# Optimization experiments

Hardware: AMD Instinct MI355X
Metric: run time of the kernel (lower is better)

## Reference

```python
import jax, jax.numpy as jnp
import numpy as np

B, L, H, NH, HD, M, NL, V, RD, NS = 4, 512, 768, 12, 64, 3072, 6, 32000, 128, 2
EPS = 1e-12
COEF = 1.0 / float(np.sqrt(HD))
NEG_INF = float('-inf')


def _ln(x, scale, bias):
    x = x - jnp.mean(x, axis=-1, keepdims=True)
    x = x * jax.lax.rsqrt(jnp.mean(jnp.square(x), axis=-1, keepdims=True) + EPS)
    return x * scale + bias


def setup_inputs() -> dict:
    key = jax.random.key(0)
    ks = jax.random.split(key, 16)
    def p(k, shape):
        return jax.random.normal(k, shape, jnp.float32) * 0.02
    return dict(
        token_ids=jax.random.randint(ks[0], (B, L), 0, V, jnp.int32),
        segment_ids=jax.random.randint(ks[1], (B, L), 0, NS, jnp.int32),
        input_mask=jnp.ones((B, L), jnp.int32),
        tok_emb=p(ks[2], (V, H)),
        seg_emb=p(ks[3], (NS, H)),
        emb_scale=jnp.ones((H,), jnp.float32),
        emb_bias=jnp.zeros((H,), jnp.float32),
        Wq=p(ks[4], (NL, H, NH, HD)), bq=jnp.zeros((NL, NH, HD), jnp.float32),
        Wk=p(ks[5], (NL, H, NH, HD)), bk=jnp.zeros((NL, NH, HD), jnp.float32),
        Wv=p(ks[6], (NL, H, NH, HD)), bv=jnp.zeros((NL, NH, HD), jnp.float32),
        relpos=p(ks[7], (NL, 2 * RD - 1, H)),
        Wo=p(ks[8], (NL, NH, HD, H)), bo=jnp.zeros((NL, H), jnp.float32),
        ln1_s=jnp.ones((NL, H), jnp.float32), ln1_b=jnp.zeros((NL, H), jnp.float32),
        W1=p(ks[9], (NL, H, M)), b1=jnp.zeros((NL, M), jnp.float32),
        W2=p(ks[10], (NL, M, H)), b2=jnp.zeros((NL, H), jnp.float32),
        ln2_s=jnp.ones((NL, H), jnp.float32), ln2_b=jnp.zeros((NL, H), jnp.float32),
    )


def _encoder(token_ids, segment_ids, input_mask,
             tok_emb, seg_emb, emb_scale, emb_bias,
             Wq, bq, Wk, bk, Wv, bv, relpos, Wo, bo,
             ln1_s, ln1_b, W1, b1, W2, b2, ln2_s, ln2_b):
    # Embedding block: token + segment embeddings, layer norm (dropout = eval/no-op)
    x = tok_emb[token_ids] + seg_emb[segment_ids]            # [B, L, H]
    x = _ln(x, emb_scale, emb_bias)
    mask = jnp.where(input_mask.astype(bool), 0.0, NEG_INF)[:, None, None, :]  # [B,1,1,L]

    for i in range(NL):
        # --- relative-position self-attention ---
        q = jnp.einsum('bqe,ehd->bqhd', x, Wq[i]) + bq[i]
        k = jnp.einsum('bke,ehd->bkhd', x, Wk[i]) + bk[i]
        v = jnp.einsum('bke,ehd->bkhd', x, Wv[i]) + bv[i]
        att = jnp.einsum('bqhd,bkhd->bhqk', q, k) + mask      # [B,NH,L,L]
        # skew trick: embed absolute [L,L] scores into relative [L, 2L-1] layout
        att = jnp.pad(att, [(0, 0), (0, 0), (0, 0), (0, L - 2)], constant_values=NEG_INF)
        att = att.reshape(att.shape[:2] + (L * (2 * L - 2),))
        att = jnp.pad(att, [(0, 0), (0, 0), (L - 1, 1)], constant_values=NEG_INF)
        att = att.reshape(att.shape[:2] + (L, 2 * L - 1))     # [B,NH,L,2L-1]
        # relative-position key/value embeddings, edge-padded to 2L-1 rows
        pad = L - RD
        rel_emb = jnp.pad(relpos[i], [(pad, pad), (0, 0)], mode='edge')  # [2L-1, H]
        k_rel = jnp.einsum('re,ehd->rhd', rel_emb, Wk[i]) + bk[i]
        att = (att + jnp.einsum('bqhd,rhd->bhqr', q, k_rel)) * COEF
        probs = jax.nn.softmax(att, axis=-1)                  # [B,NH,L,2L-1]
        v_rel = jnp.einsum('re,ehd->rhd', rel_emb, Wv[i]) + bv[i]
        rel_ctx = jnp.einsum('bhqr,rhd->bqhd', probs, v_rel)
        # un-skew probs back to [B,NH,L,L] for the absolute-position context
        p = probs.reshape(probs.shape[:2] + (L * (2 * L - 1),))[:, :, L - 1:-1]
        p = p.reshape(probs.shape[:2] + (L, 2 * L - 2))[:, :, :, :L]
        ctx = jnp.einsum('bhqk,bkhd->bqhd', p, v) + rel_ctx
        y = jnp.einsum('bqhd,hde->bqe', ctx, Wo[i]) + bo[i]
        x = _ln(x + y, ln1_s[i], ln1_b[i])
        # --- MLP block ---
        y = jax.nn.gelu(jnp.einsum('bqe,em->bqm', x, W1[i]) + b1[i])
        y = jnp.einsum('bqm,me->bqe', y, W2[i]) + b2[i]
        x = _ln(x + y, ln2_s[i], ln2_b[i])
    return x


def reference(token_ids, segment_ids, input_mask,
              tok_emb, seg_emb, emb_scale, emb_bias,
              Wq, bq, Wk, bk, Wv, bv, relpos, Wo, bo,
              ln1_s, ln1_b, W1, b1, W2, b2, ln2_s, ln2_b):
    return _encoder(token_ids, segment_ids, input_mask,
                    tok_emb, seg_emb, emb_scale, emb_bias,
                    Wq, bq, Wk, bk, Wv, bv, relpos, Wo, bo,
                    ln1_s, ln1_b, W1, b1, W2, b2, ln2_s, ln2_b)
```

## Files before the change

kernel.cpp:

```cpp
#include <hip/hip_runtime.h>
#include <hip/hip_bf16.h>
#include <math.h>

#define B_   4
#define L_   512
#define H_   768
#define NH_  12
#define HD_  64
#define M_   3072
#define NL_  6
#define RD_  128
#define NR_  255
#define ROWS (B_*L_)
#define MEXT 2304
#define COEF_ 0.125f

typedef __attribute__((ext_vector_type(8))) short bf16x8;
typedef __attribute__((ext_vector_type(4))) float f32x4;


static __device__ __forceinline__ float wave_reduce_sum(float v) {
#pragma unroll
    for (int off = 32; off > 0; off >>= 1) v += __shfl_xor(v, off, 64);
    return v;
}

static __device__ __forceinline__ float gelu_f(float x) {
    float x3 = x * x * x;
    return 0.5f * x * (1.f + tanhf(0.7978845608028654f * (x + 0.044715f * x3)));
}

static __device__ __forceinline__ unsigned short f2bfu(float v) {
    __hip_bfloat16 h = __float2bfloat16(v);
    return *(unsigned short*)&h;
}

static __device__ __forceinline__ float bfu2f(unsigned short u) {
    union { float f; unsigned int i; } x;
    x.i = ((unsigned int)u) << 16;
    return x.f;
}

static __device__ __forceinline__ void gload16(const void* g, void* l) {
    __builtin_amdgcn_global_load_lds(
        (const __attribute__((address_space(1))) void*)g,
        (__attribute__((address_space(3))) void*)l,
        16, 0, 0);
}


__global__ __launch_bounds__(256) void embed_ln_kernel(
    const int* __restrict__ tok, const int* __restrict__ seg,
    const float* __restrict__ temb, const float* __restrict__ semb,
    const float* __restrict__ sc, const float* __restrict__ bi,
    float* __restrict__ out, __hip_bfloat16* __restrict__ outb)
{
    int row = blockIdx.x;
    int t = threadIdx.x;
    int tid = tok[row], sid = seg[row];
    const float* tp = temb + (size_t)tid * H_;
    const float* sp = semb + (size_t)sid * H_;
    float v[3];
#pragma unroll
    for (int j = 0; j < 3; j++) { int idx = t + j * 256; v[j] = tp[idx] + sp[idx]; }

    __shared__ float red[4];
    __shared__ float bc;
    int lane = t & 63, wid = t >> 6;

    float s = v[0] + v[1] + v[2];
    s = wave_reduce_sum(s);
    if (lane == 0) red[wid] = s;
    __syncthreads();
    if (t == 0) bc = (red[0] + red[1] + red[2] + red[3]) * (1.f / H_);
    __syncthreads();
    float mean = bc;

    float c[3]; float ss = 0.f;
#pragma unroll
    for (int j = 0; j < 3; j++) { c[j] = v[j] - mean; ss += c[j] * c[j]; }
    ss = wave_reduce_sum(ss);
    __syncthreads();
    if (lane == 0) red[wid] = ss;
    __syncthreads();
    if (t == 0) bc = rsqrtf((red[0] + red[1] + red[2] + red[3]) * (1.f / H_) + 1e-12f);
    __syncthreads();
    float r = bc;
#pragma unroll
    for (int j = 0; j < 3; j++) {
        int idx = t + j * 256;
        float o = c[j] * r * sc[idx] + bi[idx];
        out[(size_t)row * H_ + idx] = o;
        outb[(size_t)row * H_ + idx] = __float2bfloat16(o);
    }
}


__global__ __launch_bounds__(256) void add_ln_kernel(
    const float* __restrict__ x, const float* __restrict__ p0,
    const float* __restrict__ p1, const float* __restrict__ p2,
    const float* __restrict__ bias,
    const float* __restrict__ sc, const float* __restrict__ bi,
    float* __restrict__ out, __hip_bfloat16* __restrict__ outb)
{
    int row = blockIdx.x;
    int t = threadIdx.x;
    const float* xp = x + (size_t)row * H_;
    const float* q0 = p0 + (size_t)row * H_;
    const float* q1 = p1 ? p1 + (size_t)row * H_ : nullptr;
    const float* q2 = p2 ? p2 + (size_t)row * H_ : nullptr;
    float v[3];
#pragma unroll
    for (int j = 0; j < 3; j++) {
        int idx = t + j * 256;
        float a = xp[idx] + q0[idx];
        if (q1) a += q1[idx];
        if (q2) a += q2[idx];
        if (bias) a += bias[idx];
        v[j] = a;
    }

    __shared__ float red[4];
    __shared__ float bc;
    int lane = t & 63, wid = t >> 6;

    float s = v[0] + v[1] + v[2];
    s = wave_reduce_sum(s);
    if (lane == 0) red[wid] = s;
    __syncthreads();
    if (t == 0) bc = (red[0] + red[1] + red[2] + red[3]) * (1.f / H_);
    __syncthreads();
    float mean = bc;

    float c[3]; float ss = 0.f;
#pragma unroll
    for (int j = 0; j < 3; j++) { c[j] = v[j] - mean; ss += c[j] * c[j]; }
    ss = wave_reduce_sum(ss);
    __syncthreads();
    if (lane == 0) red[wid] = ss;
    __syncthreads();
    if (t == 0) bc = rsqrtf((red[0] + red[1] + red[2] + red[3]) * (1.f / H_) + 1e-12f);
    __syncthreads();
    float r = bc;
#pragma unroll
    for (int j = 0; j < 3; j++) {
        int idx = t + j * 256;
        float o = c[j] * r * sc[idx] + bi[idx];
        out[(size_t)row * H_ + idx] = o;
        if (outb) outb[(size_t)row * H_ + idx] = __float2bfloat16(o);
    }
}


__global__ __launch_bounds__(256) void pack_layer_kernel(
    const float* __restrict__ wq, const float* __restrict__ wk, const float* __restrict__ wv,
    const float* __restrict__ wo, const float* __restrict__ w1, const float* __restrict__ w2,
    const float* __restrict__ bqL, const float* __restrict__ bkL, const float* __restrict__ bvL,
    const float* __restrict__ relL,
    __hip_bfloat16* __restrict__ WtQ, __hip_bfloat16* __restrict__ WtO,
    __hip_bfloat16* __restrict__ WtW1, __hip_bfloat16* __restrict__ WtW2,
    float* __restrict__ qkvbias, __hip_bfloat16* __restrict__ relb)
{
    const int z = blockIdx.z;
    const int t = threadIdx.x;
    if (z == 6) {
        int id = blockIdx.y * 96 + blockIdx.x;
        if (id < 765) {
            int i = id * 256 + t;
            relb[i] = __float2bfloat16(relL[i]);
        } else if (id < 774) {
            int i = (id - 765) * 256 + t;
            if (i < 2304)
                qkvbias[i] = i < 768 ? bqL[i] : (i < 1536 ? bkL[i - 768] : bvL[i - 1536]);
        }
        return;
    }
    const float* in; __hip_bfloat16* out; int K, N;
    int bx = blockIdx.x, by = blockIdx.y;
    if (z < 4) {
        if (bx >= 24) return;
        K = 768; N = 768;
        in = (z == 0) ? wq : (z == 1) ? wk : (z == 2) ? wv : wo;
        out = (z < 3) ? WtQ + (size_t)z * H_ * H_ : WtO;
    } else if (z == 4) {
        K = 768; N = 3072; in = w1; out = WtW1;
    } else {
        K = 3072; N = 768; in = w2; out = WtW2;
        int tmp = bx; bx = by; by = tmp;
    }
    __shared__ float tile[32][33];
    int bX = bx * 32, bY = by * 32;
    int tx = t & 31, ty = t >> 5;
#pragma unroll
    for (int i = 0; i < 4; i++)
        tile[ty + 8 * i][tx] = in[(size_t)(bY + ty + 8 * i) * N + bX + tx];
    __syncthreads();
#pragma unroll
    for (int i = 0; i < 4; i++)
        out[(size_t)(bX + ty + 8 * i) * K + bY + tx] = __float2bfloat16(tile[tx][ty + 8 * i]);
}


__global__ __launch_bounds__(256) void transpose_vvr_kernel(
    const __hip_bfloat16* __restrict__ qkvb,
    __hip_bfloat16* __restrict__ vT, __hip_bfloat16* __restrict__ vrT)
{
    __shared__ unsigned short tile[64][72];
    const int bx = blockIdx.x;
    const int h  = blockIdx.y;
    const int t = threadIdx.x;
    const int r = t >> 2, c0 = (t & 3) * 16;
    if (bx < 32) {
        const int kb = bx * 64;
        const unsigned short* src = (const unsigned short*)qkvb + (size_t)(kb + r) * 2304 + 1536 + h * 64 + c0;
        *(uint4*)&tile[r][c0]     = *(const uint4*)src;
        *(uint4*)&tile[r][c0 + 8] = *(const uint4*)(src + 8);
        __syncthreads();
        unsigned short outv[16];
#pragma unroll
        for (int i = 0; i < 16; i++) outv[i] = tile[c0 + i][r];
        unsigned short* dst = (unsigned short*)vT +
            ((size_t)((kb >> 9) * NH_ + h) * 64 + r) * 512 + (kb & 511) + c0;
        *(uint4*)dst       = *(uint4*)&outv[0];
        *(uint4*)(dst + 8) = *(uint4*)&outv[8];
    } else {
        const int jb = (bx - 32) * 64;
        const int j = jb + r;
        if (j < NR_) {
            const unsigned short* src = (const unsigned short*)qkvb + (size_t)(2048 + j) * 2304 + 1536 + h * 64 + c0;
            *(uint4*)&tile[r][c0]     = *(const uint4*)src;
            *(uint4*)&tile[r][c0 + 8] = *(const uint4*)(src + 8);
        } else {
#pragma unroll
            for (int i = 0; i < 16; i++) tile[r][c0 + i] = 0;
        }
        __syncthreads();
        unsigned short outv[16];
#pragma unroll
        for (int i = 0; i < 16; i++) outv[i] = tile[c0 + i][r];
        unsigned short* dst = (unsigned short*)vrT + ((size_t)(h * 64) + r) * 256 + jb + c0;
        *(uint4*)dst       = *(uint4*)&outv[0];
        *(uint4*)(dst + 8) = *(uint4*)&outv[8];
    }
}


#define TK 64

__global__ __launch_bounds__(512, 6) void gemm_bf16_kernel(
    const __hip_bfloat16* __restrict__ A, const __hip_bfloat16* __restrict__ Bt,
    const float* __restrict__ bias, float* __restrict__ Cf, __hip_bfloat16* __restrict__ Cb,
    float* __restrict__ CfX, size_t xstride,
    int M, int N, int K, int act, int ksplit)
{
    __shared__ __hip_bfloat16 As[2][128 * TK];
    __shared__ __hip_bfloat16 Bs[2][64 * TK];
    const int t = threadIdx.x;
    const int lane = t & 63;
    const int wid = t >> 6;
    const int lq = lane & 15, lg = lane >> 4;
    const int wm = (wid & 3) * 32, wn = (wid >> 2) * 32;

    const int nbx = gridDim.x;
    const int nwg = nbx * gridDim.y;
    int wgid = blockIdx.y * nbx + blockIdx.x;
    if ((nwg & 7) == 0) { int qq = nwg >> 3; wgid = (wgid & 7) * qq + (wgid >> 3); }
    const int bm = (wgid / nbx) * 128, bn = (wgid % nbx) * 64;
    const int kbase = blockIdx.z * ksplit;

    f32x4 acc[2][2];
#pragma unroll
    for (int i = 0; i < 2; i++)
#pragma unroll
        for (int j = 0; j < 2; j++) acc[i][j] = (f32x4){0.f, 0.f, 0.f, 0.f};

    const int rl = t >> 3;
    const int cswz = (((t & 7) * 16) ^ ((rl & 7) << 4)) >> 1;
    const __hip_bfloat16* ga[2];
    const __hip_bfloat16* gb;
    int lofsA[2], lofsB;
#pragma unroll
    for (int c = 0; c < 2; c++) {
        int rowa = bm + c * 64 + rl; if (rowa >= M) rowa = M - 1;
        ga[c] = A + (size_t)rowa * K + kbase + cswz;
        lofsA[c] = (c * 64 + wid * 8) * TK;
    }
    gb = Bt + (size_t)(bn + rl) * K + kbase + cswz;
    lofsB = (wid * 8) * TK;

    const int nt = ksplit / TK;
    gload16(ga[0], &As[0][lofsA[0]]);
    gload16(ga[1], &As[0][lofsA[1]]);
    gload16(gb,    &Bs[0][lofsB]);
    __syncthreads();

    int cur = 0;
    for (int kt = 0; kt < nt; kt++) {
        if (kt + 1 < nt) {
            const int koff = (kt + 1) * TK;
            gload16(ga[0] + koff, &As[cur ^ 1][lofsA[0]]);
            gload16(ga[1] + koff, &As[cur ^ 1][lofsA[1]]);
            gload16(gb + koff,    &Bs[cur ^ 1][lofsB]);
        }
#pragma unroll
        for (int kh = 0; kh < 2; kh++) {
            const int kb = kh * 64 + lg * 16;
            bf16x8 af[2], bfr[2];
#pragma unroll
            for (int i = 0; i < 2; i++) {
                int ra = wm + i * 16 + lq;
                af[i] = *(const bf16x8*)((const char*)&As[cur][0] + ra * 128 + (kb ^ ((ra & 7) << 4)));
            }
#pragma unroll
            for (int j = 0; j < 2; j++) {
                int rb = wn + j * 16 + lq;
                bfr[j] = *(const bf16x8*)((const char*)&Bs[cur][0] + rb * 128 + (kb ^ ((rb & 7) << 4)));
            }
#pragma unroll
            for (int i = 0; i < 2; i++)
#pragma unroll
                for (int j = 0; j < 2; j++)
                    acc[i][j] = __builtin_amdgcn_mfma_f32_16x16x32_bf16(af[i], bfr[j], acc[i][j], 0, 0, 0);
        }
        __syncthreads();
        cur ^= 1;
    }

    float* outf = (blockIdx.z == 0) ? Cf : (CfX + (size_t)(blockIdx.z - 1) * xstride);
#pragma unroll
    for (int i = 0; i < 2; i++) {
#pragma unroll
        for (int j = 0; j < 2; j++) {
            int col = bn + wn + j * 16 + lq;
            float bsv = bias ? bias[col] : 0.f;
            int row0 = bm + wm + i * 16 + lg * 4;
#pragma unroll
            for (int rr = 0; rr < 4; rr++) {
                int row = row0 + rr;
                if (row >= M) continue;
                float v = acc[i][j][rr] + bsv;
                if (act) v = gelu_f(v);
                if (Cb && blockIdx.z == 0) Cb[(size_t)row * N + col] = __float2bfloat16(v);
                else                       outf[(size_t)row * N + col] = v;
            }
        }
    }
}


#define PS_LD 520
#define PR_LD 264

__global__ __launch_bounds__(256, 3) void attn_kernel(
    const __hip_bfloat16* __restrict__ qkvb,
    const __hip_bfloat16* __restrict__ vT,
    const __hip_bfloat16* __restrict__ vrT,
    const int* __restrict__ mask,
    __hip_bfloat16* __restrict__ ctxb)
{
    __shared__ unsigned short RqPrel[32 * PR_LD];
    __shared__ unsigned short Ps[32 * PS_LD];
    __shared__ float mstat[32 * 4];
    __shared__ float sstat[32 * 4];
    __shared__ float maskb[512];

    const int i_ = blockIdx.x;
    const int c_ = i_ & 7, s_ = i_ >> 3;
    const int p_ = c_ + 8 * (s_ >> 4);
    const int qt = s_ & 15;
    const int b = p_ / 12, h = p_ % 12;

    const int t = threadIdx.x;
    const int lane = t & 63, w = t >> 6;
    const int lq = lane & 15, lg = lane >> 4;

    maskb[t]       = mask[b * L_ + t]       ? 0.f : -1e30f;
    maskb[t + 256] = mask[b * L_ + t + 256] ? 0.f : -1e30f;

    const char* Qbase  = (const char*)qkvb + ((size_t)(b * L_ + qt * 32) * 2304 + h * 64) * 2;
    const char* Kbase  = (const char*)qkvb + ((size_t)(b * L_) * 2304 + 768 + h * 64) * 2;
    const char* KRbase = (const char*)qkvb + ((size_t)2048 * 2304 + 768 + h * 64) * 2;

    bf16x8 afq[2][2];
#pragma unroll
    for (int ks = 0; ks < 2; ks++) {
        const int kofs = ks * 64 + lg * 16;
        afq[ks][0] = *(const bf16x8*)(Qbase + (size_t)lq * 4608 + kofs);
        afq[ks][1] = *(const bf16x8*)(Qbase + (size_t)(16 + lq) * 4608 + kofs);
    }

    {
        f32x4 accr[2][4];
#pragma unroll
        for (int i = 0; i < 2; i++)
#pragma unroll
            for (int j = 0; j < 4; j++) accr[i][j] = (f32x4){0.f, 0.f, 0.f, 0.f};
#pragma unroll
        for (int ks = 0; ks < 2; ks++) {
            const int kofs = ks * 64 + lg * 16;
            bf16x8 bkr_[4];
#pragma unroll
            for (int jt = 0; jt < 4; jt++) {
                int j = w * 64 + jt * 16 + lq;
                int jr = j > 254 ? 254 : j;
                bkr_[jt] = *(const bf16x8*)(KRbase + (size_t)jr * 4608 + kofs);
            }
#pragma unroll
            for (int jt = 0; jt < 4; jt++) {
                accr[0][jt] = __builtin_amdgcn_mfma_f32_16x16x32_bf16(afq[ks][0], bkr_[jt], accr[0][jt], 0, 0, 0);
                accr[1][jt] = __builtin_amdgcn_mfma_f32_16x16x32_bf16(afq[ks][1], bkr_[jt], accr[1][jt], 0, 0, 0);
            }
        }
#pragma unroll
        for (int it = 0; it < 2; it++)
#pragma unroll
            for (int jt = 0; jt < 4; jt++)
#pragma unroll
                for (int r = 0; r < 4; r++)
                    RqPrel[(it * 16 + lg * 4 + r) * PR_LD + w * 64 + jt * 16 + lq] = f2bfu(accr[it][jt][r]);
    }
    __syncthreads();

    f32x4 accs[2][8];
#pragma unroll
    for (int i = 0; i < 2; i++)
#pragma unroll
        for (int j = 0; j < 8; j++) accs[i][j] = (f32x4){0.f, 0.f, 0.f, 0.f};
#pragma unroll
    for (int ks = 0; ks < 2; ks++) {
        const int kofs = ks * 64 + lg * 16;
        bf16x8 bk_[8];
#pragma unroll
        for (int jt = 0; jt < 8; jt++) {
            int key = w * 128 + jt * 16 + lq;
            bk_[jt] = *(const bf16x8*)(Kbase + (size_t)key * 4608 + kofs);
        }
#pragma unroll
        for (int jt = 0; jt < 8; jt++) {
            accs[0][jt] = __builtin_amdgcn_mfma_f32_16x16x32_bf16(afq[ks][0], bk_[jt], accs[0][jt], 0, 0, 0);
            accs[1][jt] = __builtin_amdgcn_mfma_f32_16x16x32_bf16(afq[ks][1], bk_[jt], accs[1][jt], 0, 0, 0);
        }
    }

#pragma unroll
    for (int it = 0; it < 2; it++) {
#pragma unroll
        for (int r = 0; r < 4; r++) {
            int q = it * 16 + lg * 4 + r;
            int qg = qt * 32 + q;
            float mx = -INFINITY;
#pragma unroll
            for (int jt = 0; jt < 8; jt++) {
                int k = w * 128 + jt * 16 + lq;
                int jc = k - qg + 127;
                jc = jc < 0 ? 0 : (jc > 254 ? 254 : jc);
                float s = (accs[it][jt][r] + bfu2f(RqPrel[q * PR_LD + jc])) * COEF_ + maskb[k];
                accs[it][jt][r] = s;
                mx = fmaxf(mx, s);
            }
#pragma unroll
            for (int off = 1; off < 16; off <<= 1) mx = fmaxf(mx, __shfl_xor(mx, off, 64));
            if (lq == 0) mstat[q * 4 + w] = mx;
        }
    }
    __syncthreads();

#pragma unroll
    for (int it = 0; it < 2; it++) {
#pragma unroll
        for (int r = 0; r < 4; r++) {
            int q = it * 16 + lg * 4 + r;
            float4 mv = *(const float4*)&mstat[q * 4];
            float gm = fmaxf(fmaxf(mv.x, mv.y), fmaxf(mv.z, mv.w));
            float ssum = 0.f;
#pragma unroll
            for (int jt = 0; jt < 8; jt++) {
                int k = w * 128 + jt * 16 + lq;
                float p = __expf(accs[it][jt][r] - gm);
                ssum += p;
                Ps[q * PS_LD + k] = f2bfu(p);
            }
#pragma unroll
            for (int off = 1; off < 16; off <<= 1) ssum += __shfl_xor(ssum, off, 64);
            if (lq == 0) sstat[q * 4 + w] = ssum;
        }
    }
    __syncthreads();

    const __hip_bfloat16* vTb  = vT  + (((size_t)(b * NH_ + h) * 64) + w * 16 + lq) * 512 + lg * 8;
    const __hip_bfloat16* vrTb = vrT + ((size_t)(h * 64) + w * 16 + lq) * 256 + lg * 8;
    bf16x8 bvpre[8], vrpre[8];
#pragma unroll
    for (int ks = 0; ks < 8; ks++) {
        bvpre[ks] = *(const bf16x8*)(vTb + ks * 32);
        vrpre[ks] = *(const bf16x8*)(vrTb + ks * 32);
    }
    {
        int q = t >> 3, sub = t & 7;
        int qg = qt * 32 + q;
#pragma unroll
        for (int jj = 0; jj < 32; jj++) {
            int j = sub + 8 * jj;
            if (j == 0 || j == 254) continue;
            if (j == 255) { RqPrel[q * PR_LD + 255] = 0; continue; }
            int k = qg + j - 127;
            unsigned short val = ((unsigned)k < 512u) ? Ps[q * PS_LD + k] : (unsigned short)0;
            RqPrel[q * PR_LD + j] = val;
        }
    }
    {
        int task = t >> 2, ts = t & 3;
        int q = task >> 1, side = task & 1;
        int qg = qt * 32 + q;
        float sum = 0.f;
        if (side == 0) {
            int hi = qg - 127;
            for (int k = ts; k <= hi; k += 4) sum += bfu2f(Ps[q * PS_LD + k]);
        } else {
            for (int k = qg + 127 + ts; k < 512; k += 4) sum += bfu2f(Ps[q * PS_LD + k]);
        }
        sum += __shfl_xor(sum, 1, 64);
        sum += __shfl_xor(sum, 2, 64);
        if (ts == 0) RqPrel[q * PR_LD + (side == 0 ? 0 : 254)] = f2bfu(sum);
    }
    __syncthreads();

    f32x4 accv[2];
    accv[0] = (f32x4){0.f, 0.f, 0.f, 0.f};
    accv[1] = (f32x4){0.f, 0.f, 0.f, 0.f};

#pragma unroll
    for (int ks = 0; ks < 8; ks++) {
        bf16x8 pa0 = *(const bf16x8*)((const char*)Ps + (size_t)lq * (PS_LD * 2) + ks * 64 + lg * 16);
        bf16x8 pa1 = *(const bf16x8*)((const char*)Ps + (size_t)(16 + lq) * (PS_LD * 2) + ks * 64 + lg * 16);
        accv[0] = __builtin_amdgcn_mfma_f32_16x16x32_bf16(pa0, bvpre[ks], accv[0], 0, 0, 0);
        accv[1] = __builtin_amdgcn_mfma_f32_16x16x32_bf16(pa1, bvpre[ks], accv[1], 0, 0, 0);
    }
#pragma unroll
    for (int ks = 8; ks < 16; ks++) {
        bf16x8 bv = *(const bf16x8*)(vTb + ks * 32);
        bf16x8 pa0 = *(const bf16x8*)((const char*)Ps + (size_t)lq * (PS_LD * 2) + ks * 64 + lg * 16);
        bf16x8 pa1 = *(const bf16x8*)((const char*)Ps + (size_t)(16 + lq) * (PS_LD * 2) + ks * 64 + lg * 16);
        accv[0] = __builtin_amdgcn_mfma_f32_16x16x32_bf16(pa0, bv, accv[0], 0, 0, 0);
        accv[1] = __builtin_amdgcn_mfma_f32_16x16x32_bf16(pa1, bv, accv[1], 0, 0, 0);
    }
#pragma unroll
    for (int ks = 0; ks < 8; ks++) {
        bf16x8 pa0 = *(const bf16x8*)((const char*)RqPrel + (size_t)lq * (PR_LD * 2) + ks * 64 + lg * 16);
        bf16x8 pa1 = *(const bf16x8*)((const char*)RqPrel + (size_t)(16 + lq) * (PR_LD * 2) + ks * 64 + lg * 16);
        accv[0] = __builtin_amdgcn_mfma_f32_16x16x32_bf16(pa0, vrpre[ks], accv[0], 0, 0, 0);
        accv[1] = __builtin_amdgcn_mfma_f32_16x16x32_bf16(pa1, vrpre[ks], accv[1], 0, 0, 0);
    }

#pragma unroll
    for (int it = 0; it < 2; it++) {
#pragma unroll
        for (int r = 0; r < 4; r++) {
            int q = it * 16 + lg * 4 + r;
            float4 sv = *(const float4*)&sstat[q * 4];
            float inv = 1.f / (sv.x + sv.y + sv.z + sv.w);
            ctxb[(size_t)(b * L_ + qt * 32 + q) * 768 + h * 64 + w * 16 + lq] =
                __float2bfloat16(accv[it][r] * inv);
        }
    }
}


extern "C" void kernel_launch(void* const* d_in, const int* in_sizes, int n_in,
                              void* d_out, int out_size, void* d_ws, size_t ws_size,
                              hipStream_t stream)
{
    const int*   tok    = (const int*)d_in[0];
    const int*   seg    = (const int*)d_in[1];
    const int*   maskp  = (const int*)d_in[2];
    const float* temb   = (const float*)d_in[3];
    const float* semb   = (const float*)d_in[4];
    const float* esc    = (const float*)d_in[5];
    const float* ebi    = (const float*)d_in[6];
    const float* Wq     = (const float*)d_in[7];
    const float* bq     = (const float*)d_in[8];
    const float* Wk     = (const float*)d_in[9];
    const float* bk     = (const float*)d_in[10];
    const float* Wv     = (const float*)d_in[11];
    const float* bv     = (const float*)d_in[12];
    const float* relpos = (const float*)d_in[13];
    const float* Wo     = (const float*)d_in[14];
    const float* bo     = (const float*)d_in[15];
    const float* ln1s   = (const float*)d_in[16];
    const float* ln1b   = (const float*)d_in[17];
    const float* W1     = (const float*)d_in[18];
    const float* b1     = (const float*)d_in[19];
    const float* W2     = (const float*)d_in[20];
    const float* b2     = (const float*)d_in[21];
    const float* ln2s   = (const float*)d_in[22];
    const float* ln2b   = (const float*)d_in[23];

    const size_t NX = (size_t)ROWS * H_;
    float* x       = (float*)d_ws;
    float* x2      = x + NX;
    float* y       = x2 + NX;
    float* qkvbias = y + NX;
    __hip_bfloat16* xb    = (__hip_bfloat16*)(qkvbias + 2304);
    __hip_bfloat16* x2b   = xb    + (size_t)MEXT * H_;
    __hip_bfloat16* ctxb  = x2b   + NX;
    __hip_bfloat16* qkvb  = ctxb  + NX;
    __hip_bfloat16* vT    = qkvb  + (size_t)MEXT * 2304;
    __hip_bfloat16* vrT   = vT    + (size_t)B_ * NH_ * 64 * 512;
    __hip_bfloat16* WtQ   = vrT   + (size_t)NH_ * 64 * 256;
    __hip_bfloat16* WtO   = WtQ   + (size_t)2304 * H_;
    __hip_bfloat16* WtW1  = WtO   + (size_t)H_ * H_;
    __hip_bfloat16* WtW2  = WtW1  + (size_t)M_ * H_;
    __hip_bfloat16* h1b   = WtW2  + (size_t)H_ * M_;

    float* spill = (float*)qkvb;

    dim3 blk(256);
    dim3 blk512(512);

    embed_ln_kernel<<<ROWS, blk, 0, stream>>>(tok, seg, temb, semb, esc, ebi, x, xb);

    for (int l = 0; l < NL_; l++) {
        const float* wq = Wq + (size_t)l * H_ * H_;
        const float* wk = Wk + (size_t)l * H_ * H_;
        const float* wv = Wv + (size_t)l * H_ * H_;
        const float* wo = Wo + (size_t)l * H_ * H_;
        const float* w1 = W1 + (size_t)l * H_ * M_;
        const float* w2 = W2 + (size_t)l * M_ * H_;

        pack_layer_kernel<<<dim3(96, 24, 7), blk, 0, stream>>>(
            wq, wk, wv, wo, w1, w2,
            bq + (size_t)l * H_, bk + (size_t)l * H_, bv + (size_t)l * H_,
            relpos + (size_t)l * NR_ * H_,
            WtQ, WtO, WtW1, WtW2, qkvbias, xb + (size_t)ROWS * H_);

        gemm_bf16_kernel<<<dim3(36, 18), blk512, 0, stream>>>(xb, WtQ, qkvbias, nullptr, qkvb, nullptr, 0,
                                                              MEXT, 2304, H_, 0, H_);
        transpose_vvr_kernel<<<dim3(36, 12), blk, 0, stream>>>(qkvb, vT, vrT);

        attn_kernel<<<dim3(768), blk, 0, stream>>>(qkvb, vT, vrT, maskp, ctxb);

        gemm_bf16_kernel<<<dim3(12, 16, 2), blk512, 0, stream>>>(ctxb, WtO, nullptr, y, nullptr, spill, NX,
                                                                 ROWS, H_, H_, 0, 384);
        add_ln_kernel<<<ROWS, blk, 0, stream>>>(x, y, spill, nullptr, bo + (size_t)l * H_,
                                                ln1s + (size_t)l * H_, ln1b + (size_t)l * H_, x2, x2b);

        gemm_bf16_kernel<<<dim3(48, 16), blk512, 0, stream>>>(x2b, WtW1, b1 + (size_t)l * M_, nullptr, h1b, nullptr, 0,
                                                              ROWS, M_, H_, 1, H_);
        gemm_bf16_kernel<<<dim3(12, 16, 3), blk512, 0, stream>>>(h1b, WtW2, nullptr, y, nullptr, spill, NX,
                                                                 ROWS, H_, M_, 0, 1024);

        float* outp = (l == NL_ - 1) ? (float*)d_out : x;
        __hip_bfloat16* outbp = (l == NL_ - 1) ? nullptr : xb;
        add_ln_kernel<<<ROWS, blk, 0, stream>>>(x2, y, spill, spill + NX, b2 + (size_t)l * H_,
                                                ln2s + (size_t)l * H_, ln2b + (size_t)l * H_, outp, outbp);
    }
}
```

Baseline: 732.0 us.

## Split attention block across eight waves instead of four

Raises the attention kernel from 256 to 512 threads per block and repartitions every phase over eight waves: each wave covers half as many keys and relative positions in the score stage. In the PV stage the waves split into two query halves by four head-dim slices, so each wave keeps a single accumulator. Softmax statistics grow to eight partials per query row, and the gather and boundary-sum loops are respread over the extra threads. The aim is more latency hiding per block and less register pressure per thread, at the cost of more shared-memory traffic for the partial statistics. It also risks lower occupancy if register or LDS limits keep only a few large blocks per CU.

Result: slower. 802.7 us (+9.7%).

```diff
diff --git a/kernel.cpp b/kernel.cpp
--- a/kernel.cpp
+++ b/kernel.cpp
@@ -351,7 +351,7 @@
 #define PS_LD 520
 #define PR_LD 264
 
-__global__ __launch_bounds__(256, 3) void attn_kernel(
+__global__ __launch_bounds__(512, 4) void attn_kernel(
     const __hip_bfloat16* __restrict__ qkvb,
     const __hip_bfloat16* __restrict__ vT,
     const __hip_bfloat16* __restrict__ vrT,
@@ -360,8 +360,8 @@
 {
     __shared__ unsigned short RqPrel[32 * PR_LD];
     __shared__ unsigned short Ps[32 * PS_LD];
-    __shared__ float mstat[32 * 4];
-    __shared__ float sstat[32 * 4];
+    __shared__ float mstat[32 * 8];
+    __shared__ float sstat[32 * 8];
     __shared__ float maskb[512];
 
     const int i_ = blockIdx.x;
@@ -374,8 +374,7 @@
     const int lane = t & 63, w = t >> 6;
     const int lq = lane & 15, lg = lane >> 4;
 
-    maskb[t]       = mask[b * L_ + t]       ? 0.f : -1e30f;
-    maskb[t + 256] = mask[b * L_ + t + 256] ? 0.f : -1e30f;
+    maskb[t] = mask[b * L_ + t] ? 0.f : -1e30f;
 
     const char* Qbase  = (const char*)qkvb + ((size_t)(b * L_ + qt * 32) * 2304 + h * 64) * 2;
     const char* Kbase  = (const char*)qkvb + ((size_t)(b * L_) * 2304 + 768 + h * 64) * 2;
@@ -390,23 +389,23 @@
     }
 
     {
-        f32x4 accr[2][4];
+        f32x4 accr[2][2];
 #pragma unroll
         for (int i = 0; i < 2; i++)
 #pragma unroll
-            for (int j = 0; j < 4; j++) accr[i][j] = (f32x4){0.f, 0.f, 0.f, 0.f};
+            for (int j = 0; j < 2; j++) accr[i][j] = (f32x4){0.f, 0.f, 0.f, 0.f};
 #pragma unroll
         for (int ks = 0; ks < 2; ks++) {
             const int kofs = ks * 64 + lg * 16;
-            bf16x8 bkr_[4];
-#pragma unroll
-            for (int jt = 0; jt < 4; jt++) {
-                int j = w * 64 + jt * 16 + lq;
+            bf16x8 bkr_[2];
+#pragma unroll
+            for (int jt = 0; jt < 2; jt++) {
+                int j = w * 32 + jt * 16 + lq;
                 int jr = j > 254 ? 254 : j;
                 bkr_[jt] = *(const bf16x8*)(KRbase + (size_t)jr * 4608 + kofs);
             }
 #pragma unroll
-            for (int jt = 0; jt < 4; jt++) {
+            for (int jt = 0; jt < 2; jt++) {
                 accr[0][jt] = __builtin_amdgcn_mfma_f32_16x16x32_bf16(afq[ks][0], bkr_[jt], accr[0][jt], 0, 0, 0);
                 accr[1][jt] = __builtin_amdgcn_mfma_f32_16x16x32_bf16(afq[ks][1], bkr_[jt], accr[1][jt], 0, 0, 0);
             }
@@ -414,29 +413,29 @@
 #pragma unroll
         for (int it = 0; it < 2; it++)
 #pragma unroll
-            for (int jt = 0; jt < 4; jt++)
+            for (int jt = 0; jt < 2; jt++)
 #pragma unroll
                 for (int r = 0; r < 4; r++)
-                    RqPrel[(it * 16 + lg * 4 + r) * PR_LD + w * 64 + jt * 16 + lq] = f2bfu(accr[it][jt][r]);
-    }
-    __syncthreads();
-
-    f32x4 accs[2][8];
+                    RqPrel[(it * 16 + lg * 4 + r) * PR_LD + w * 32 + jt * 16 + lq] = f2bfu(accr[it][jt][r]);
+    }
+    __syncthreads();
+
+    f32x4 accs[2][4];
 #pragma unroll
     for (int i = 0; i < 2; i++)
 #pragma unroll
-        for (int j = 0; j < 8; j++) accs[i][j] = (f32x4){0.f, 0.f, 0.f, 0.f};
+        for (int j = 0; j < 4; j++) accs[i][j] = (f32x4){0.f, 0.f, 0.f, 0.f};
 #pragma unroll
     for (int ks = 0; ks < 2; ks++) {
         const int kofs = ks * 64 + lg * 16;
-        bf16x8 bk_[8];
-#pragma unroll
-        for (int jt = 0; jt < 8; jt++) {
-            int key = w * 128 + jt * 16 + lq;
+        bf16x8 bk_[4];
+#pragma unroll
+        for (int jt = 0; jt < 4; jt++) {
+            int key = w * 64 + jt * 16 + lq;
             bk_[jt] = *(const bf16x8*)(Kbase + (size_t)key * 4608 + kofs);
         }
 #pragma unroll
-        for (int jt = 0; jt < 8; jt++) {
+        for (int jt = 0; jt < 4; jt++) {
             accs[0][jt] = __builtin_amdgcn_mfma_f32_16x16x32_bf16(afq[ks][0], bk_[jt], accs[0][jt], 0, 0, 0);
             accs[1][jt] = __builtin_amdgcn_mfma_f32_16x16x32_bf16(afq[ks][1], bk_[jt], accs[1][jt], 0, 0, 0);
         }
@@ -450,8 +449,8 @@
             int qg = qt * 32 + q;
             float mx = -INFINITY;
 #pragma unroll
-            for (int jt = 0; jt < 8; jt++) {
-                int k = w * 128 + jt * 16 + lq;
+            for (int jt = 0; jt < 4; jt++) {
+                int k = w * 64 + jt * 16 + lq;
                 int jc = k - qg + 127;
                 jc = jc < 0 ? 0 : (jc > 254 ? 254 : jc);
                 float s = (accs[it][jt][r] + bfu2f(RqPrel[q * PR_LD + jc])) * COEF_ + maskb[k];
@@ -460,7 +459,7 @@
             }
 #pragma unroll
             for (int off = 1; off < 16; off <<= 1) mx = fmaxf(mx, __shfl_xor(mx, off, 64));
-            if (lq == 0) mstat[q * 4 + w] = mx;
+            if (lq == 0) mstat[q * 8 + w] = mx;
         }
     }
     __syncthreads();
@@ -470,25 +469,28 @@
 #pragma unroll
         for (int r = 0; r < 4; r++) {
             int q = it * 16 + lg * 4 + r;
-            float4 mv = *(const float4*)&mstat[q * 4];
-            float gm = fmaxf(fmaxf(mv.x, mv.y), fmaxf(mv.z, mv.w));
+            float4 m0 = *(const float4*)&mstat[q * 8];
+            float4 m1 = *(const float4*)&mstat[q * 8 + 4];
+            float gm = fmaxf(fmaxf(fmaxf(m0.x, m0.y), fmaxf(m0.z, m0.w)),
+                             fmaxf(fmaxf(m1.x, m1.y), fmaxf(m1.z, m1.w)));
             float ssum = 0.f;
 #pragma unroll
-            for (int jt = 0; jt < 8; jt++) {
-                int k = w * 128 + jt * 16 + lq;
+            for (int jt = 0; jt < 4; jt++) {
+                int k = w * 64 + jt * 16 + lq;
                 float p = __expf(accs[it][jt][r] - gm);
                 ssum += p;
                 Ps[q * PS_LD + k] = f2bfu(p);
             }
 #pragma unroll
             for (int off = 1; off < 16; off <<= 1) ssum += __shfl_xor(ssum, off, 64);
-            if (lq == 0) sstat[q * 4 + w] = ssum;
-        }
-    }
-    __syncthreads();
-
-    const __hip_bfloat16* vTb  = vT  + (((size_t)(b * NH_ + h) * 64) + w * 16 + lq) * 512 + lg * 8;
-    const __hip_bfloat16* vrTb = vrT + ((size_t)(h * 64) + w * 16 + lq) * 256 + lg * 8;
+            if (lq == 0) sstat[q * 8 + w] = ssum;
+        }
+    }
+    __syncthreads();
+
+    const int hq = w >> 2, ds = (w & 3) * 16;
+    const __hip_bfloat16* vTb  = vT  + (((size_t)(b * NH_ + h) * 64) + ds + lq) * 512 + lg * 8;
+    const __hip_bfloat16* vrTb = vrT + ((size_t)(h * 64) + ds + lq) * 256 + lg * 8;
     bf16x8 bvpre[8], vrpre[8];
 #pragma unroll
     for (int ks = 0; ks < 8; ks++) {
@@ -496,11 +498,11 @@
         vrpre[ks] = *(const bf16x8*)(vrTb + ks * 32);
     }
     {
-        int q = t >> 3, sub = t & 7;
+        int q = t >> 4, sub = t & 15;
         int qg = qt * 32 + q;
 #pragma unroll
-        for (int jj = 0; jj < 32; jj++) {
-            int j = sub + 8 * jj;
+        for (int jj = 0; jj < 16; jj++) {
+            int j = sub + 16 * jj;
             if (j == 0 || j == 254) continue;
             if (j == 255) { RqPrel[q * PR_LD + 255] = 0; continue; }
             int k = qg + j - 127;
@@ -509,59 +511,51 @@
         }
     }
     {
-        int task = t >> 2, ts = t & 3;
+        int task = t >> 3, ts = t & 7;
         int q = task >> 1, side = task & 1;
         int qg = qt * 32 + q;
         float sum = 0.f;
         if (side == 0) {
             int hi = qg - 127;
-            for (int k = ts; k <= hi; k += 4) sum += bfu2f(Ps[q * PS_LD + k]);
+            for (int k = ts; k <= hi; k += 8) sum += bfu2f(Ps[q * PS_LD + k]);
         } else {
-            for (int k = qg + 127 + ts; k < 512; k += 4) sum += bfu2f(Ps[q * PS_LD + k]);
+            for (int k = qg + 127 + ts; k < 512; k += 8) sum += bfu2f(Ps[q * PS_LD + k]);
         }
         sum += __shfl_xor(sum, 1, 64);
         sum += __shfl_xor(sum, 2, 64);
+        sum += __shfl_xor(sum, 4, 64);
         if (ts == 0) RqPrel[q * PR_LD + (side == 0 ? 0 : 254)] = f2bfu(sum);
     }
     __syncthreads();
 
-    f32x4 accv[2];
-    accv[0] = (f32x4){0.f, 0.f, 0.f, 0.f};
-    accv[1] = (f32x4){0.f, 0.f, 0.f, 0.f};
+    f32x4 accv = (f32x4){0.f, 0.f, 0.f, 0.f};
+    const int parow = hq * 16 + lq;
 
 #pragma unroll
     for (int ks = 0; ks < 8; ks++) {
-        bf16x8 pa0 = *(const bf16x8*)((const char*)Ps + (size_t)lq * (PS_LD * 2) + ks * 64 + lg * 16);
-        bf16x8 pa1 = *(const bf16x8*)((const char*)Ps + (size_t)(16 + lq) * (PS_LD * 2) + ks * 64 + lg * 16);
-        accv[0] = __builtin_amdgcn_mfma_f32_16x16x32_bf16(pa0, bvpre[ks], accv[0], 0, 0, 0);
-        accv[1] = __builtin_amdgcn_mfma_f32_16x16x32_bf16(pa1, bvpre[ks], accv[1], 0, 0, 0);
+        bf16x8 pa = *(const bf16x8*)((const char*)Ps + (size_t)parow * (PS_LD * 2) + ks * 64 + lg * 16);
+        accv = __builtin_amdgcn_mfma_f32_16x16x32_bf16(pa, bvpre[ks], accv, 0, 0, 0);
     }
 #pragma unroll
     for (int ks = 8; ks < 16; ks++) {
         bf16x8 bv = *(const bf16x8*)(vTb + ks * 32);
-        bf16x8 pa0 = *(const bf16x8*)((const char*)Ps + (size_t)lq * (PS_LD * 2) + ks * 64 + lg * 16);
-        bf16x8 pa1 = *(const bf16x8*)((const char*)Ps + (size_t)(16 + lq) * (PS_LD * 2) + ks * 64 + lg * 16);
-        accv[0] = __builtin_amdgcn_mfma_f32_16x16x32_bf16(pa0, bv, accv[0], 0, 0, 0);
-        accv[1] = __builtin_amdgcn_mfma_f32_16x16x32_bf16(pa1, bv, accv[1], 0, 0, 0);
+        bf16x8 pa = *(const bf16x8*)((const char*)Ps + (size_t)parow * (PS_LD * 2) + ks * 64 + lg * 16);
+        accv = __builtin_amdgcn_mfma_f32_16x16x32_bf16(pa, bv, accv, 0, 0, 0);
     }
 #pragma unroll
     for (int ks = 0; ks < 8; ks++) {
-        bf16x8 pa0 = *(const bf16x8*)((const char*)RqPrel + (size_t)lq * (PR_LD * 2) + ks * 64 + lg * 16);
-        bf16x8 pa1 = *(const bf16x8*)((const char*)RqPrel + (size_t)(16 + lq) * (PR_LD * 2) + ks * 64 + lg * 16);
-        accv[0] = __builtin_amdgcn_mfma_f32_16x16x32_bf16(pa0, vrpre[ks], accv[0], 0, 0, 0);
-        accv[1] = __builtin_amdgcn_mfma_f32_16x16x32_bf16(pa1, vrpre[ks], accv[1], 0, 0, 0);
-    }
-
-#pragma unroll
-    for (int it = 0; it < 2; it++) {
-#pragma unroll
-        for (int r = 0; r < 4; r++) {
-            int q = it * 16 + lg * 4 + r;
-            float4 sv = *(const float4*)&sstat[q * 4];
-            float inv = 1.f / (sv.x + sv.y + sv.z + sv.w);
-            ctxb[(size_t)(b * L_ + qt * 32 + q) * 768 + h * 64 + w * 16 + lq] =
-                __float2bfloat16(accv[it][r] * inv);
-        }
+        bf16x8 pa = *(const bf16x8*)((const char*)RqPrel + (size_t)parow * (PR_LD * 2) + ks * 64 + lg * 16);
+        accv = __builtin_amdgcn_mfma_f32_16x16x32_bf16(pa, vrpre[ks], accv, 0, 0, 0);
+    }
+
+#pragma unroll
+    for (int r = 0; r < 4; r++) {
+        int q = hq * 16 + lg * 4 + r;
+        float4 s0 = *(const float4*)&sstat[q * 8];
+        float4 s1 = *(const float4*)&sstat[q * 8 + 4];
+        float inv = 1.f / (s0.x + s0.y + s0.z + s0.w + s1.x + s1.y + s1.z + s1.w);
+        ctxb[(size_t)(b * L_ + qt * 32 + q) * 768 + h * 64 + ds + lq] =
+            __float2bfloat16(accv[r] * inv);
     }
 }
 
@@ -637,7 +631,7 @@
                                                               MEXT, 2304, H_, 0, H_);
         transpose_vvr_kernel<<<dim3(36, 12), blk, 0, stream>>>(qkvb, vT, vrT);
 
-        attn_kernel<<<dim3(768), blk, 0, stream>>>(qkvb, vT, vrT, maskp, ctxb);
+        attn_kernel<<<dim3(768), blk512, 0, stream>>>(qkvb, vT, vrT, maskp, ctxb);
 
         gemm_bf16_kernel<<<dim3(12, 16, 2), blk512, 0, stream>>>(ctxb, WtO, nullptr, y, nullptr, spill, NX,
                                                                  ROWS, H_, H_, 0, 384);
```

## Pack all layer weights in one launch and reorder attention loads for overlap

Applied to the files above, without the earlier changes.

The six per-layer weight pack/transpose launches become a single launch that converts every layer's weights, biases and relpos tables into per-layer bf16 buffers up front. The QKV GEMM now reads relpos rows through a second A pointer, so they no longer have to be copied into the tail of xb. In the attention kernel the key and value-rel loads are issued earlier, and one barrier is removed so the relative-score MFMAs overlap with the key-score loads. This costs more workspace memory for six layers of packed weights and keeps more registers live in the attention kernel.

Result: slower. 756.1 us (+3.3%).

```diff
diff --git a/kernel.cpp b/kernel.cpp
--- a/kernel.cpp
+++ b/kernel.cpp
@@ -152,40 +152,51 @@
 }
 
 
-__global__ __launch_bounds__(256) void pack_layer_kernel(
-    const float* __restrict__ wq, const float* __restrict__ wk, const float* __restrict__ wv,
-    const float* __restrict__ wo, const float* __restrict__ w1, const float* __restrict__ w2,
-    const float* __restrict__ bqL, const float* __restrict__ bkL, const float* __restrict__ bvL,
-    const float* __restrict__ relL,
-    __hip_bfloat16* __restrict__ WtQ, __hip_bfloat16* __restrict__ WtO,
-    __hip_bfloat16* __restrict__ WtW1, __hip_bfloat16* __restrict__ WtW2,
-    float* __restrict__ qkvbias, __hip_bfloat16* __restrict__ relb)
+__global__ __launch_bounds__(256) void pack_all_kernel(
+    const float* __restrict__ Wq, const float* __restrict__ Wk, const float* __restrict__ Wv,
+    const float* __restrict__ Wo, const float* __restrict__ W1, const float* __restrict__ W2,
+    const float* __restrict__ bq, const float* __restrict__ bk, const float* __restrict__ bv,
+    const float* __restrict__ relpos,
+    __hip_bfloat16* __restrict__ WtQ6, __hip_bfloat16* __restrict__ WtO6,
+    __hip_bfloat16* __restrict__ WtW16, __hip_bfloat16* __restrict__ WtW26,
+    float* __restrict__ qkvbias6, __hip_bfloat16* __restrict__ relb6)
 {
-    const int z = blockIdx.z;
+    const int l = blockIdx.z / 7;
+    const int zz = blockIdx.z % 7;
     const int t = threadIdx.x;
-    if (z == 6) {
+    if (zz == 6) {
         int id = blockIdx.y * 96 + blockIdx.x;
         if (id < 765) {
             int i = id * 256 + t;
-            relb[i] = __float2bfloat16(relL[i]);
+            relb6[(size_t)l * NR_ * H_ + i] = __float2bfloat16(relpos[(size_t)l * NR_ * H_ + i]);
         } else if (id < 774) {
             int i = (id - 765) * 256 + t;
-            if (i < 2304)
-                qkvbias[i] = i < 768 ? bqL[i] : (i < 1536 ? bkL[i - 768] : bvL[i - 1536]);
+            if (i < 2304) {
+                float v = i < 768 ? bq[(size_t)l * H_ + i]
+                        : (i < 1536 ? bk[(size_t)l * H_ + i - 768]
+                                    : bv[(size_t)l * H_ + i - 1536]);
+                qkvbias6[(size_t)l * 2304 + i] = v;
+            }
         }
         return;
     }
     const float* in; __hip_bfloat16* out; int K, N;
     int bx = blockIdx.x, by = blockIdx.y;
-    if (z < 4) {
+    if (zz < 4) {
         if (bx >= 24) return;
         K = 768; N = 768;
-        in = (z == 0) ? wq : (z == 1) ? wk : (z == 2) ? wv : wo;
-        out = (z < 3) ? WtQ + (size_t)z * H_ * H_ : WtO;
-    } else if (z == 4) {
-        K = 768; N = 3072; in = w1; out = WtW1;
+        in = (zz == 0) ? Wq + (size_t)l * H_ * H_
+           : (zz == 1) ? Wk + (size_t)l * H_ * H_
+           : (zz == 2) ? Wv + (size_t)l * H_ * H_
+                       : Wo + (size_t)l * H_ * H_;
+        out = (zz < 3) ? WtQ6 + (size_t)l * 3 * H_ * H_ + (size_t)zz * H_ * H_
+                       : WtO6 + (size_t)l * H_ * H_;
+    } else if (zz == 4) {
+        K = 768; N = 3072;
+        in = W1 + (size_t)l * H_ * M_; out = WtW16 + (size_t)l * M_ * H_;
     } else {
-        K = 3072; N = 768; in = w2; out = WtW2;
+        K = 3072; N = 768;
+        in = W2 + (size_t)l * M_ * H_; out = WtW26 + (size_t)l * H_ * M_;
         int tmp = bx; bx = by; by = tmp;
     }
     __shared__ float tile[32][33];
@@ -248,7 +259,8 @@
 #define TK 64
 
 __global__ __launch_bounds__(512, 6) void gemm_bf16_kernel(
-    const __hip_bfloat16* __restrict__ A, const __hip_bfloat16* __restrict__ Bt,
+    const __hip_bfloat16* __restrict__ A, const __hip_bfloat16* __restrict__ A2,
+    const __hip_bfloat16* __restrict__ Bt,
     const float* __restrict__ bias, float* __restrict__ Cf, __hip_bfloat16* __restrict__ Cb,
     float* __restrict__ CfX, size_t xstride,
     int M, int N, int K, int act, int ksplit)
@@ -281,8 +293,16 @@
     int lofsA[2], lofsB;
 #pragma unroll
     for (int c = 0; c < 2; c++) {
-        int rowa = bm + c * 64 + rl; if (rowa >= M) rowa = M - 1;
-        ga[c] = A + (size_t)rowa * K + kbase + cswz;
+        int rowa = bm + c * 64 + rl;
+        const __hip_bfloat16* base;
+        if (A2 && rowa >= ROWS) {
+            int rr = rowa - ROWS; if (rr > NR_ - 1) rr = NR_ - 1;
+            base = A2 + (size_t)rr * K;
+        } else {
+            if (rowa >= M) rowa = M - 1;
+            base = A + (size_t)rowa * K;
+        }
+        ga[c] = base + kbase + cswz;
         lofsA[c] = (c * 64 + wid * 8) * TK;
     }
     gb = Bt + (size_t)(bn + rl) * K + kbase + cswz;
@@ -389,58 +409,68 @@
         afq[ks][1] = *(const bf16x8*)(Qbase + (size_t)(16 + lq) * 4608 + kofs);
     }
 
-    {
-        f32x4 accr[2][4];
-#pragma unroll
-        for (int i = 0; i < 2; i++)
-#pragma unroll
-            for (int j = 0; j < 4; j++) accr[i][j] = (f32x4){0.f, 0.f, 0.f, 0.f};
-#pragma unroll
-        for (int ks = 0; ks < 2; ks++) {
-            const int kofs = ks * 64 + lg * 16;
-            bf16x8 bkr_[4];
-#pragma unroll
-            for (int jt = 0; jt < 4; jt++) {
-                int j = w * 64 + jt * 16 + lq;
-                int jr = j > 254 ? 254 : j;
-                bkr_[jt] = *(const bf16x8*)(KRbase + (size_t)jr * 4608 + kofs);
-            }
-#pragma unroll
-            for (int jt = 0; jt < 4; jt++) {
-                accr[0][jt] = __builtin_amdgcn_mfma_f32_16x16x32_bf16(afq[ks][0], bkr_[jt], accr[0][jt], 0, 0, 0);
-                accr[1][jt] = __builtin_amdgcn_mfma_f32_16x16x32_bf16(afq[ks][1], bkr_[jt], accr[1][jt], 0, 0, 0);
-            }
-        }
-#pragma unroll
-        for (int it = 0; it < 2; it++)
-#pragma unroll
-            for (int jt = 0; jt < 4; jt++)
-#pragma unroll
-                for (int r = 0; r < 4; r++)
-                    RqPrel[(it * 16 + lg * 4 + r) * PR_LD + w * 64 + jt * 16 + lq] = f2bfu(accr[it][jt][r]);
-    }
-    __syncthreads();
-
-    f32x4 accs[2][8];
+    f32x4 accr[2][4];
 #pragma unroll
     for (int i = 0; i < 2; i++)
 #pragma unroll
-        for (int j = 0; j < 8; j++) accs[i][j] = (f32x4){0.f, 0.f, 0.f, 0.f};
+        for (int j = 0; j < 4; j++) accr[i][j] = (f32x4){0.f, 0.f, 0.f, 0.f};
 #pragma unroll
     for (int ks = 0; ks < 2; ks++) {
         const int kofs = ks * 64 + lg * 16;
-        bf16x8 bk_[8];
-#pragma unroll
-        for (int jt = 0; jt < 8; jt++) {
-            int key = w * 128 + jt * 16 + lq;
-            bk_[jt] = *(const bf16x8*)(Kbase + (size_t)key * 4608 + kofs);
-        }
-#pragma unroll
-        for (int jt = 0; jt < 8; jt++) {
-            accs[0][jt] = __builtin_amdgcn_mfma_f32_16x16x32_bf16(afq[ks][0], bk_[jt], accs[0][jt], 0, 0, 0);
-            accs[1][jt] = __builtin_amdgcn_mfma_f32_16x16x32_bf16(afq[ks][1], bk_[jt], accs[1][jt], 0, 0, 0);
-        }
-    }
+        bf16x8 bkr_[4];
+#pragma unroll
+        for (int jt = 0; jt < 4; jt++) {
+            int j = w * 64 + jt * 16 + lq;
+            int jr = j > 254 ? 254 : j;
+            bkr_[jt] = *(const bf16x8*)(KRbase + (size_t)jr * 4608 + kofs);
+        }
+#pragma unroll
+        for (int jt = 0; jt < 4; jt++) {
+            accr[0][jt] = __builtin_amdgcn_mfma_f32_16x16x32_bf16(afq[ks][0], bkr_[jt], accr[0][jt], 0, 0, 0);
+            accr[1][jt] = __builtin_amdgcn_mfma_f32_16x16x32_bf16(afq[ks][1], bkr_[jt], accr[1][jt], 0, 0, 0);
+        }
+    }
+
+    bf16x8 bk0_[8], bk1_[8];
+#pragma unroll
+    for (int jt = 0; jt < 8; jt++) {
+        int key = w * 128 + jt * 16 + lq;
+        bk0_[jt] = *(const bf16x8*)(Kbase + (size_t)key * 4608 + lg * 16);
+        bk1_[jt] = *(const bf16x8*)(Kbase + (size_t)key * 4608 + 64 + lg * 16);
+    }
+
+#pragma unroll
+    for (int it = 0; it < 2; it++)
+#pragma unroll
+        for (int jt = 0; jt < 4; jt++)
+#pragma unroll
+            for (int r = 0; r < 4; r++)
+                RqPrel[(it * 16 + lg * 4 + r) * PR_LD + w * 64 + jt * 16 + lq] = f2bfu(accr[it][jt][r]);
+
+    f32x4 accs[2][8];
+#pragma unroll
+    for (int i = 0; i < 2; i++)
+#pragma unroll
+        for (int j = 0; j < 8; j++) accs[i][j] = (f32x4){0.f, 0.f, 0.f, 0.f};
+#pragma unroll
+    for (int jt = 0; jt < 8; jt++) {
+        accs[0][jt] = __builtin_amdgcn_mfma_f32_16x16x32_bf16(afq[0][0], bk0_[jt], accs[0][jt], 0, 0, 0);
+        accs[1][jt] = __builtin_amdgcn_mfma_f32_16x16x32_bf16(afq[0][1], bk0_[jt], accs[1][jt], 0, 0, 0);
+    }
+#pragma unroll
+    for (int jt = 0; jt < 8; jt++) {
+        accs[0][jt] = __builtin_amdgcn_mfma_f32_16x16x32_bf16(afq[1][0], bk1_[jt], accs[0][jt], 0, 0, 0);
+        accs[1][jt] = __builtin_amdgcn_mfma_f32_16x16x32_bf16(afq[1][1], bk1_[jt], accs[1][jt], 0, 0, 0);
+    }
+
+    const __hip_bfloat16* vTb  = vT  + (((size_t)(b * NH_ + h) * 64) + w * 16 + lq) * 512 + lg * 8;
+    const __hip_bfloat16* vrTb = vrT + ((size_t)(h * 64) + w * 16 + lq) * 256 + lg * 8;
+    bf16x8 vrpre[8];
+#pragma unroll
+    for (int ks = 0; ks < 8; ks++)
+        vrpre[ks] = *(const bf16x8*)(vrTb + ks * 32);
+
+    __syncthreads();
 
 #pragma unroll
     for (int it = 0; it < 2; it++) {
@@ -487,14 +517,10 @@
     }
     __syncthreads();
 
-    const __hip_bfloat16* vTb  = vT  + (((size_t)(b * NH_ + h) * 64) + w * 16 + lq) * 512 + lg * 8;
-    const __hip_bfloat16* vrTb = vrT + ((size_t)(h * 64) + w * 16 + lq) * 256 + lg * 8;
-    bf16x8 bvpre[8], vrpre[8];
-#pragma unroll
-    for (int ks = 0; ks < 8; ks++) {
+    bf16x8 bvpre[8];
+#pragma unroll
+    for (int ks = 0; ks < 8; ks++)
         bvpre[ks] = *(const bf16x8*)(vTb + ks * 32);
-        vrpre[ks] = *(const bf16x8*)(vrTb + ks * 32);
-    }
     {
         int q = t >> 3, sub = t & 7;
         int qg = qt * 32 + q;
@@ -596,21 +622,22 @@
     const float* ln2b   = (const float*)d_in[23];
 
     const size_t NX = (size_t)ROWS * H_;
-    float* x       = (float*)d_ws;
-    float* x2      = x + NX;
-    float* y       = x2 + NX;
-    float* qkvbias = y + NX;
-    __hip_bfloat16* xb    = (__hip_bfloat16*)(qkvbias + 2304);
-    __hip_bfloat16* x2b   = xb    + (size_t)MEXT * H_;
+    float* x        = (float*)d_ws;
+    float* x2       = x + NX;
+    float* y        = x2 + NX;
+    float* qkvbias6 = y + NX;
+    __hip_bfloat16* xb    = (__hip_bfloat16*)(qkvbias6 + 6 * 2304);
+    __hip_bfloat16* x2b   = xb    + NX;
     __hip_bfloat16* ctxb  = x2b   + NX;
     __hip_bfloat16* qkvb  = ctxb  + NX;
     __hip_bfloat16* vT    = qkvb  + (size_t)MEXT * 2304;
     __hip_bfloat16* vrT   = vT    + (size_t)B_ * NH_ * 64 * 512;
-    __hip_bfloat16* WtQ   = vrT   + (size_t)NH_ * 64 * 256;
-    __hip_bfloat16* WtO   = WtQ   + (size_t)2304 * H_;
-    __hip_bfloat16* WtW1  = WtO   + (size_t)H_ * H_;
-    __hip_bfloat16* WtW2  = WtW1  + (size_t)M_ * H_;
-    __hip_bfloat16* h1b   = WtW2  + (size_t)H_ * M_;
+    __hip_bfloat16* relb6 = vrT   + (size_t)NH_ * 64 * 256;
+    __hip_bfloat16* WtQ6  = relb6 + (size_t)NL_ * NR_ * H_;
+    __hip_bfloat16* WtO6  = WtQ6  + (size_t)NL_ * 2304 * H_;
+    __hip_bfloat16* WtW16 = WtO6  + (size_t)NL_ * H_ * H_;
+    __hip_bfloat16* WtW26 = WtW16 + (size_t)NL_ * M_ * H_;
+    __hip_bfloat16* h1b   = WtW26 + (size_t)NL_ * H_ * M_;
 
     float* spill = (float*)qkvb;
 
@@ -618,35 +645,36 @@
     dim3 blk512(512);
 
     embed_ln_kernel<<<ROWS, blk, 0, stream>>>(tok, seg, temb, semb, esc, ebi, x, xb);
+    pack_all_kernel<<<dim3(96, 24, NL_ * 7), blk, 0, stream>>>(
+        Wq, Wk, Wv, Wo, W1, W2, bq, bk, bv, relpos,
+        WtQ6, WtO6, WtW16, WtW26, qkvbias6, relb6);
 
     for (int l = 0; l < NL_; l++) {
-        const float* wq = Wq + (size_t)l * H_ * H_;
-        const float* wk = Wk + (size_t)l * H_ * H_;
-        const float* wv = Wv + (size_t)l * H_ * H_;
-        const float* wo = Wo + (size_t)l * H_ * H_;
-        const float* w1 = W1 + (size_t)l * H_ * M_;
-        const float* w2 = W2 + (size_t)l * M_ * H_;
-
-        pack_layer_kernel<<<dim3(96, 24, 7), blk, 0, stream>>>(
-            wq, wk, wv, wo, w1, w2,
-            bq + (size_t)l * H_, bk + (size_t)l * H_, bv + (size_t)l * H_,
-            relpos + (size_t)l * NR_ * H_,
-            WtQ, WtO, WtW1, WtW2, qkvbias, xb + (size_t)ROWS * H_);
-
-        gemm_bf16_kernel<<<dim3(36, 18), blk512, 0, stream>>>(xb, WtQ, qkvbias, nullptr, qkvb, nullptr, 0,
+        __hip_bfloat16* WtQ  = WtQ6  + (size_t)l * 2304 * H_;
+        __hip_bfloat16* WtO  = WtO6  + (size_t)l * H_ * H_;
+        __hip_bfloat16* WtW1 = WtW16 + (size_t)l * M_ * H_;
+        __hip_bfloat16* WtW2 = WtW26 + (size_t)l * H_ * M_;
+        __hip_bfloat16* relb = relb6 + (size_t)l * NR_ * H_;
+        float* qkvbias = qkvbias6 + (size_t)l * 2304;
+
+        gemm_bf16_kernel<<<dim3(36, 18), blk512, 0, stream>>>(xb, relb, WtQ, qkvbias,
+                                                              nullptr, qkvb, nullptr, 0,
                                                               MEXT, 2304, H_, 0, H_);
         transpose_vvr_kernel<<<dim3(36, 12), blk, 0, stream>>>(qkvb, vT, vrT);
 
         attn_kernel<<<dim3(768), blk, 0, stream>>>(qkvb, vT, vrT, maskp, ctxb);
 
-        gemm_bf16_kernel<<<dim3(12, 16, 2), blk512, 0, stream>>>(ctxb, WtO, nullptr, y, nullptr, spill, NX,
+        gemm_bf16_kernel<<<dim3(12, 16, 2), blk512, 0, stream>>>(ctxb, nullptr, WtO, nullptr,
+                                                                 y, nullptr, spill, NX,
                                                                  ROWS, H_, H_, 0, 384);
         add_ln_kernel<<<ROWS, blk, 0, stream>>>(x, y, spill, nullptr, bo + (size_t)l * H_,
                                                 ln1s + (size_t)l * H_, ln1b + (size_t)l * H_, x2, x2b);
 
-        gemm_bf16_kernel<<<dim3(48, 16), blk512, 0, stream>>>(x2b, WtW1, b1 + (size_t)l * M_, nullptr, h1b, nullptr, 0,
+        gemm_bf16_kernel<<<dim3(48, 16), blk512, 0, stream>>>(x2b, nullptr, WtW1, b1 + (size_t)l * M_,
+                                                              nullptr, h1b, nullptr, 0,
                                                               ROWS, M_, H_, 1, H_);
-        gemm_bf16_kernel<<<dim3(12, 16, 3), blk512, 0, stream>>>(h1b, WtW2, nullptr, y, nullptr, spill, NX,
+        gemm_bf16_kernel<<<dim3(12, 16, 3), blk512, 0, stream>>>(h1b, nullptr, WtW2, nullptr,
+                                                                 y, nullptr, spill, NX,
                                                                  ROWS, H_, M_, 0, 1024);
 
         float* outp = (l == NL_ - 1) ? (float*)d_out : x;
```
